# Kernel optimization log

Hardware: AMD Instinct MI355X
Metric: run time of the kernel (lower is better)

Reference implementation:

```python
import jax, jax.numpy as jnp
import numpy as np

N = 192            # image grid size (NxN)
N_SHOTS = 192
N_SAMPLES = 192
TWO_PI = 2.0 * np.pi
PIPE_ITERS = 3     # gpunufft default is ~10; 3 suffices for a CPU-runnable reference


def initialize_2D_radial(n_shots, n_samples):
    """Radial trajectory, k in [-0.5, 0.5), shape (n_shots*n_samples, 2)."""
    angles = np.pi * np.arange(n_shots) / n_shots
    radii = np.linspace(-0.5, 0.5, n_samples, endpoint=False)
    kx = radii[None, :] * np.cos(angles[:, None])
    ky = radii[None, :] * np.sin(angles[:, None])
    return np.stack([kx, ky], axis=-1).reshape(-1, 2).astype(np.float32)


def setup_inputs() -> dict:
    key = jax.random.key(0)
    x = jax.random.normal(key, (2, N, N), dtype=jnp.float32)  # real/imag image
    trajectory = jnp.asarray(initialize_2D_radial(N_SHOTS, N_SAMPLES))  # (M,2)
    return {"x": x, "trajectory": trajectory}


def _mats(traj):
    # Separable NDFT factors: exp(-2pi i k_x * px), exp(-2pi i k_y * py).
    # A: (M, N), B: (M, N); M*N complex64 ~= 57 MB each.
    p = jnp.arange(N, dtype=jnp.float32) - N / 2.0  # centered pixel coords
    A = jnp.exp(-1j * TWO_PI * traj[:, 0:1] * p[None, :])
    B = jnp.exp(-1j * TWO_PI * traj[:, 1:2] * p[None, :])
    return A.astype(jnp.complex64), B.astype(jnp.complex64)


def _op(img, A, B):
    # type-2 NUFFT (exact NDFT): image (N,N) -> kspace (M,)
    t = jnp.einsum('my,xy->mx', B, img)      # contract y first
    return jnp.einsum('mx,mx->m', A, t)


def _adj(d, A, B):
    # type-1 NUFFT adjoint: samples (M,) -> image (N,N)
    return jnp.einsum('mx,my->xy', jnp.conj(A) * d[:, None], jnp.conj(B))


def _pipe_density(A, B):
    # Pipe & Menon iterative density compensation: w <- w / |F F^H w|
    w = jnp.ones(A.shape[0], dtype=jnp.complex64)
    def body(i, w):
        q = _op(_adj(w, A, B), A, B)
        return w / jnp.maximum(jnp.abs(q), 1e-20)
    w = jax.lax.fori_loop(0, PIPE_ITERS, body, w)
    return jnp.abs(w)  # real positive weights


def reference(x, trajectory):
    img = (x[0] + 1j * x[1]).astype(jnp.complex64)  # (N,N) complex image
    A, B = _mats(trajectory)
    # density weights computed from detached trajectory (gpunufft init-time)
    traj_sg = jax.lax.stop_gradient(trajectory)
    Asg, Bsg = _mats(traj_sg)
    w = jax.lax.stop_gradient(_pipe_density(Asg, Bsg))
    kspace = _op(img, A, B)                       # forward NUFFT
    adjoint = _adj(w * kspace, A, B)              # density-compensated adjoint
    return jnp.stack([adjoint.real, adjoint.imag])  # (2,N,N) float32
```

## Files before the change

### kernel.cpp

```cpp
#include <hip/hip_runtime.h>
#include <math.h>


#define MTOT 36864
#define NPIX 192
#define SPLITS 128
#define MPS (MTOT / SPLITS)
#define ADJ_CHUNKS (MPS / 16)
#define PG 4

typedef __attribute__((ext_vector_type(8))) short s16x8;
typedef __attribute__((ext_vector_type(4))) float f32x4;
typedef __attribute__((ext_vector_type(4))) unsigned u32x4;

__device__ __forceinline__ f32x4 mfma_bf16(u32x4 a, u32x4 b, f32x4 c) {
    return __builtin_amdgcn_mfma_f32_16x16x32_bf16(
        __builtin_bit_cast(s16x8, a), __builtin_bit_cast(s16x8, b), c, 0, 0, 0);
}

__device__ __forceinline__ void g2l16(const void* g, void* l) {
    __builtin_amdgcn_global_load_lds(
        (const __attribute__((address_space(1))) void*)g,
        (__attribute__((address_space(3))) void*)l, 16, 0, 0);
}

__device__ __forceinline__ void split_pk(float a, float b, unsigned &hi, unsigned &lo) {
    const unsigned ua = __float_as_uint(a), ub = __float_as_uint(b);
    const unsigned ha = (ua + 0x8000u) & 0xffff0000u;
    const unsigned hb = (ub + 0x8000u) & 0xffff0000u;
    hi = (ha >> 16) | hb;
    const float la = a - __uint_as_float(ha);
    const float lb = b - __uint_as_float(hb);
    lo = ((__float_as_uint(la) + 0x8000u) >> 16) |
         ((__float_as_uint(lb) + 0x8000u) & 0xffff0000u);
}

__device__ __forceinline__ void ksplit(float k, float &kh, float &kl) {
    kh = __uint_as_float(__float_as_uint(k) & 0xfffff000u);
    kl = k - kh;
}
__device__ __forceinline__ float redphase(float kh, float kl, float p) {
    float r = kh * p;
    r -= rintf(r);
    r = fmaf(kl, p, r);
    return r;
}
__device__ __forceinline__ unsigned rot16(unsigned v) {
    return __builtin_amdgcn_alignbit(v, v, 16);
}
__device__ __forceinline__ int swz(int c) {
    return ((c ^ (c >> 2)) & 3) << 2;
}

__global__ void precompP_k(const float* __restrict__ traj, const int comp,
                           unsigned* __restrict__ PS) {
    const int m = blockIdx.x * 256 + threadIdx.x;
    const int c = blockIdx.y;
    float kh, kl; ksplit(traj[2 * m + comp], kh, kl);
    const float ph = redphase(kh, kl, (float)(c - 96));
    const float co = __builtin_amdgcn_cosf(ph);
    const float si = __builtin_amdgcn_sinf(ph);
    unsigned h, l; split_pk(co, -si, h, l);
    const int mc = m >> 4, mi = (m & 15) ^ swz(c);
    PS[(size_t)mc * 6144 + c * 16 + mi]        = h;
    PS[(size_t)mc * 6144 + 3072 + c * 16 + mi] = l;
}

__global__ void ebuild_k(const float* __restrict__ traj,
                         const float* __restrict__ dr, const float* __restrict__ di,
                         unsigned* __restrict__ ES) {
    const int m = blockIdx.x * 256 + threadIdx.x;
    const int c = blockIdx.y;
    float kh, kl; ksplit(traj[2 * m], kh, kl);
    const float ph = redphase(kh, kl, (float)(c - 96));
    const float co = __builtin_amdgcn_cosf(ph);
    const float si = __builtin_amdgcn_sinf(ph);
    const float dr_ = dr[m], di_ = di[m];
    const float Er = co * dr_ - si * di_;
    const float Ei = co * di_ + si * dr_;
    unsigned h, l; split_pk(Er, Ei, h, l);
    const int mc = m >> 4, mi = (m & 15) ^ swz(c);
    ES[(size_t)mc * 6144 + c * 16 + mi]        = h;
    ES[(size_t)mc * 6144 + 3072 + c * 16 + mi] = l;
}

__global__ void winit_k(float* __restrict__ wr, float* __restrict__ wi) {
    const int m = blockIdx.x * 256 + threadIdx.x;
    wr[m] = 1.f; wi[m] = 0.f;
}

__global__ __launch_bounds__(256) void adj_gemm_k(
    const unsigned* __restrict__ ES, const unsigned* __restrict__ BS,
    float* __restrict__ outP)
{
    __shared__ unsigned sAB[2][4096];
    const int tid = threadIdx.x;
    const int lane = tid & 63, wid = tid >> 6;
    const int l15 = lane & 15, qd = lane >> 4;
    const int L = blockIdx.x;
    const int xcd = L & 7, j = L >> 3;
    const int s = xcd * (SPLITS / 8) + j / 9;
    const int tile = j % 9;
    const int bx = tile % 3, by = tile / 3;
    const int wi = wid & 1, wj = wid >> 1;
    const int x0 = bx * 64 + wi * 32, y0 = by * 64 + wj * 32;
    float* outRe = outP + (size_t)(s & (PG - 1)) * (2 * MTOT);
    float* outIm = outRe + MTOT;

    f32x4 accRe[2][2], accIm[2][2];
    #pragma unroll
    for (int i = 0; i < 2; ++i)
        #pragma unroll
        for (int j2 = 0; j2 < 2; ++j2) {
            accRe[i][j2] = (f32x4){0.f, 0.f, 0.f, 0.f};
            accIm[i][j2] = (f32x4){0.f, 0.f, 0.f, 0.f};
        }

    const unsigned* gp[4];
    {
        const unsigned* E0 = ES + (size_t)(s * ADJ_CHUNKS) * 6144;
        const unsigned* B0 = BS + (size_t)(s * ADJ_CHUNKS) * 6144;
        gp[0] = E0 + bx * 1024 + tid * 4;
        gp[1] = E0 + 3072 + bx * 1024 + tid * 4;
        gp[2] = B0 + by * 1024 + tid * 4;
        gp[3] = B0 + 3072 + by * 1024 + tid * 4;
    }
    int eoff[2], boff[2];
    #pragma unroll
    for (int t = 0; t < 2; ++t) {
        const int cE = wi * 32 + t * 16 + l15;
        eoff[t] = cE * 16 + ((qd ^ ((cE ^ (cE >> 2)) & 3)) << 2);
        const int cB = wj * 32 + t * 16 + l15;
        boff[t] = 2048 + cB * 16 + ((qd ^ ((cB ^ (cB >> 2)) & 3)) << 2);
    }

    #pragma unroll
    for (int v = 0; v < 4; ++v)
        g2l16(gp[v], &sAB[0][v * 1024 + tid * 4]);
    __syncthreads();

    for (int ch = 0; ch < ADJ_CHUNKS; ++ch) {
        const int cur = ch & 1, nxt = cur ^ 1;
        if (ch + 1 < ADJ_CHUNKS) {
            #pragma unroll
            for (int v = 0; v < 4; ++v) {
                gp[v] += 6144;
                g2l16(gp[v], &sAB[nxt][v * 1024 + tid * 4]);
            }
        }

        u32x4 Eh[2], El[2];
        #pragma unroll
        for (int t = 0; t < 2; ++t) {
            Eh[t] = *(const u32x4*)(&sAB[cur][eoff[t]]);
            El[t] = *(const u32x4*)(&sAB[cur][1024 + eoff[t]]);
        }
        #pragma unroll
        for (int sj = 0; sj < 2; ++sj) {
            const u32x4 Ph = *(const u32x4*)(&sAB[cur][boff[sj]]);
            const u32x4 Pl = *(const u32x4*)(&sAB[cur][1024 + boff[sj]]);
            u32x4 Qh, Ql;
            #pragma unroll
            for (int r = 0; r < 4; ++r) {
                Qh[r] = rot16(Ph[r]) ^ 0x00008000u;
                Ql[r] = rot16(Pl[r]) ^ 0x00008000u;
            }
            #pragma unroll
            for (int si = 0; si < 2; ++si) {
                accRe[si][sj] = mfma_bf16(Eh[si], Ph, accRe[si][sj]);
                accRe[si][sj] = mfma_bf16(Eh[si], Pl, accRe[si][sj]);
                accRe[si][sj] = mfma_bf16(El[si], Ph, accRe[si][sj]);
                accIm[si][sj] = mfma_bf16(Eh[si], Qh, accIm[si][sj]);
                accIm[si][sj] = mfma_bf16(Eh[si], Ql, accIm[si][sj]);
                accIm[si][sj] = mfma_bf16(El[si], Qh, accIm[si][sj]);
            }
        }
        __syncthreads();
    }

    #pragma unroll
    for (int si = 0; si < 2; ++si)
        #pragma unroll
        for (int sj = 0; sj < 2; ++sj)
            #pragma unroll
            for (int rg = 0; rg < 4; ++rg) {
                const int x = x0 + si * 16 + qd * 4 + rg;
                const int y = y0 + sj * 16 + l15;
                atomicAdd(outRe + x * NPIX + y, accRe[si][sj][rg]);
                atomicAdd(outIm + x * NPIX + y, accIm[si][sj][rg]);
            }
}

__device__ __forceinline__ void fw_stage_load(const unsigned* __restrict__ Ghi,
                                              const unsigned* __restrict__ Glo,
                                              int tid, int koff, u32x4 st[3]) {
    #pragma unroll
    for (int j = 0; j < 3; ++j) {
        const int li = tid + j * 576;
        if (li < 1536) {
            const int row = li >> 3, pl = (li >> 2) & 1, qt = li & 3;
            const unsigned* src = pl ? Glo : Ghi;
            st[j] = *(const u32x4*)(src + row * 192 + koff + qt * 4);
        }
    }
}
__device__ __forceinline__ void fw_stage_write(unsigned* sb, int tid, const u32x4 st[3]) {
    #pragma unroll
    for (int j = 0; j < 3; ++j) {
        const int li = tid + j * 576;
        if (li < 1536) {
            const int row = li >> 3, pl = (li >> 2) & 1, qt = li & 3;
            *(u32x4*)(sb + pl * 3840 + row * 20 + qt * 4) = st[j];
        }
    }
}

__global__ __launch_bounds__(576) void fwdq_k(
    const float* __restrict__ traj,
    const unsigned* __restrict__ Ghi, const unsigned* __restrict__ Glo,
    float* __restrict__ wre, float* __restrict__ wim,
    const int mode,
    float* __restrict__ qre, float* __restrict__ qim)
{
    __shared__ unsigned sG[2][2 * 3840];
    const int tid = threadIdx.x;
    const int lane = tid & 63, wid = tid >> 6;
    const int l15 = lane & 15, q = lane >> 4;
    const int m = (blockIdx.x * 9 + wid) * 16 + l15;
    const float2 kk = *(const float2*)(traj + 2 * m);
    float kxh, kxl, kyh, kyl;
    ksplit(kk.x, kxh, kxl);
    ksplit(kk.y, kyh, kyl);

    f32x4 tre[12], tim[12];
    #pragma unroll
    for (int i = 0; i < 12; ++i) {
        tre[i] = (f32x4){0.f, 0.f, 0.f, 0.f};
        tim[i] = (f32x4){0.f, 0.f, 0.f, 0.f};
    }

    float bc, bs;
    { const float ph = redphase(kyh, kyl, (float)(q * 4 - 96)); 
      bc = __builtin_amdgcn_cosf(ph); bs = __builtin_amdgcn_sinf(ph); }
    const float r1c = __builtin_amdgcn_cosf(kk.y), r1s = __builtin_amdgcn_sinf(kk.y);
    float r16c, r16s;
    { float g = kk.y * 16.f; g -= rintf(g);
      r16c = __builtin_amdgcn_cosf(g); r16s = __builtin_amdgcn_sinf(g); }

    u32x4 st[3];
    fw_stage_load(Ghi, Glo, tid, 0, st);
    fw_stage_write(&sG[0][0], tid, st);
    __syncthreads();

    for (int ch = 0; ch < 12; ++ch) {
        if (ch < 11) fw_stage_load(Ghi, Glo, tid, (ch + 1) * 16, st);

        u32x4 Ph, Pl, Qh, Ql;
        {
            float c = bc, s = bs;
            #pragma unroll
            for (int r = 0; r < 4; ++r) {
                unsigned h, l; split_pk(c, s, h, l);
                Ph[r] = h; Pl[r] = l;
                Qh[r] = rot16(h) ^ 0x00008000u;
                Ql[r] = rot16(l) ^ 0x00008000u;
                const float nc = c * r1c - s * r1s, ns = s * r1c + c * r1s;
                c = nc; s = ns;
            }
            const float nbc = bc * r16c - bs * r16s, nbs = bs * r16c + bc * r16s;
            bc = nbc; bs = nbs;
        }

        const unsigned* sb = &sG[ch & 1][0];
        #pragma unroll
        for (int si = 0; si < 12; ++si) {
            const int base = (si * 16 + l15) * 20 + q * 4;
            const u32x4 gh = *(const u32x4*)(sb + base);
            const u32x4 gl = *(const u32x4*)(sb + 3840 + base);
            tre[si] = mfma_bf16(gh, Ph, tre[si]);
            tre[si] = mfma_bf16(gh, Pl, tre[si]);
            tre[si] = mfma_bf16(gl, Ph, tre[si]);
            tim[si] = mfma_bf16(gh, Qh, tim[si]);
            tim[si] = mfma_bf16(gh, Ql, tim[si]);
            tim[si] = mfma_bf16(gl, Qh, tim[si]);
        }

        if (ch < 11) {
            __syncthreads();
            fw_stage_write(&sG[(ch + 1) & 1][0], tid, st);
            __syncthreads();
        }
    }

    float qr = 0.f, qi = 0.f;
    {
        float g = kk.x * 16.f; g -= rintf(g);
        const float rc = __builtin_amdgcn_cosf(g), rs = __builtin_amdgcn_sinf(g);
        #pragma unroll
        for (int rg = 0; rg < 4; ++rg) {
            const float ph = redphase(kxh, kxl, (float)(q * 4 + rg - 96));
            float c = __builtin_amdgcn_cosf(ph), s = __builtin_amdgcn_sinf(ph);
            #pragma unroll
            for (int si = 0; si < 12; ++si) {
                const float tr = tre[si][rg], ti = tim[si][rg];
                qr += c * tr + s * ti;
                qi += c * ti - s * tr;
                const float nc = c * rc - s * rs, ns = s * rc + c * rs;
                c = nc; s = ns;
            }
        }
    }
    qr += __shfl_xor(qr, 16); qi += __shfl_xor(qi, 16);
    qr += __shfl_xor(qr, 32); qi += __shfl_xor(qi, 32);
    if (lane < 16) {
        if (mode == 0) {
            const float den = fmaxf(sqrtf(qr * qr + qi * qi), 1e-20f);
            wre[m] /= den; wim[m] /= den;
        } else {
            const float sc = sqrtf(wre[m] * wre[m] + wim[m] * wim[m]);
            qre[m] = qr * sc; qim[m] = qi * sc;
        }
    }
}

__global__ void presplit_k(const float* __restrict__ re, const float* __restrict__ im,
                           unsigned* __restrict__ Gh, unsigned* __restrict__ Gl) {
    const int e = blockIdx.x * 256 + threadIdx.x;
    unsigned h, l;
    split_pk(re[e], im[e], h, l);
    Gh[e] = h; Gl[e] = l;
}

__global__ void presplitP_k(const float* __restrict__ outP,
                            unsigned* __restrict__ Gh, unsigned* __restrict__ Gl) {
    const int e = blockIdx.x * 256 + threadIdx.x;
    float re = 0.f, im = 0.f;
    #pragma unroll
    for (int g = 0; g < PG; ++g) {
        re += outP[(size_t)g * (2 * MTOT) + e];
        im += outP[(size_t)g * (2 * MTOT) + MTOT + e];
    }
    unsigned h, l;
    split_pk(re, im, h, l);
    Gh[e] = h; Gl[e] = l;
}

__global__ void reduceOut_k(const float* __restrict__ outP, float* __restrict__ out) {
    const int e = blockIdx.x * 256 + threadIdx.x;
    float re = 0.f, im = 0.f;
    #pragma unroll
    for (int g = 0; g < PG; ++g) {
        re += outP[(size_t)g * (2 * MTOT) + e];
        im += outP[(size_t)g * (2 * MTOT) + MTOT + e];
    }
    out[e] = re; out[MTOT + e] = im;
}

extern "C" void kernel_launch(void* const* d_in, const int* in_sizes, int n_in,
                              void* d_out, int out_size, void* d_ws, size_t ws_size,
                              hipStream_t stream)
{
    const float* xin  = (const float*)d_in[0];
    const float* traj = (const float*)d_in[1];
    float* out = (float*)d_out;

    char* pb = (char*)d_ws;
    unsigned* BS = (unsigned*)pb; pb += (size_t)2304 * 6144 * 4;
    unsigned* ES = (unsigned*)pb; pb += (size_t)2304 * 6144 * 4;
    float* outP = (float*)pb; pb += (size_t)PG * 2 * MTOT * 4;
    float* wr   = (float*)pb; pb += MTOT * 4;
    float* wi   = (float*)pb; pb += MTOT * 4;
    float* dre  = (float*)pb; pb += MTOT * 4;
    float* dim_ = (float*)pb; pb += MTOT * 4;
    unsigned* Ghi = (unsigned*)pb; pb += MTOT * 4;
    unsigned* Glo = (unsigned*)pb; pb += MTOT * 4;

    precompP_k<<<dim3(MTOT / 256, NPIX), 256, 0, stream>>>(traj, 1, BS);
    winit_k<<<MTOT / 256, 256, 0, stream>>>(wr, wi);

    for (int it = 0; it < 3; ++it) {
        hipMemsetAsync(outP, 0, (size_t)PG * 2 * MTOT * 4, stream);
        ebuild_k<<<dim3(MTOT / 256, NPIX), 256, 0, stream>>>(traj, wr, wi, ES);
        adj_gemm_k<<<9 * SPLITS, 256, 0, stream>>>(ES, BS, outP);
        presplitP_k<<<MTOT / 256, 256, 0, stream>>>(outP, Ghi, Glo);
        fwdq_k<<<256, 576, 0, stream>>>(traj, Ghi, Glo, wr, wi, 0, dre, dim_);
    }

    presplit_k<<<MTOT / 256, 256, 0, stream>>>(xin, xin + MTOT, Ghi, Glo);
    fwdq_k<<<256, 576, 0, stream>>>(traj, Ghi, Glo, wr, wi, 1, dre, dim_);
    hipMemsetAsync(outP, 0, (size_t)PG * 2 * MTOT * 4, stream);
    ebuild_k<<<dim3(MTOT / 256, NPIX), 256, 0, stream>>>(traj, dre, dim_, ES);
    adj_gemm_k<<<9 * SPLITS, 256, 0, stream>>>(ES, BS, outP);
    reduceOut_k<<<MTOT / 256, 256, 0, stream>>>(outP, out);
}
```

Before: 491.2 us.

## Triple-buffer adjoint GEMM LDS tiles with explicit vmcnt waits

Moves the adjoint GEMM kernel from double-buffered to triple-buffered LDS staging, issuing global-to-LDS loads two chunks ahead. Each iteration waits only on the older loads through explicit vmcnt counts. All LDS fragments are read into registers before a second barrier, so the MFMA work runs after the buffer is released. The aim is to hide global load latency behind compute and remove the trailing full syncthreads. In exchange it uses more LDS per block, which may lower occupancy, and it relies on hand-written waitcnt values being correct.

```diff
diff --git a/kernel.cpp b/kernel.cpp
--- a/kernel.cpp
+++ b/kernel.cpp
@@ -93,7 +93,7 @@
     const unsigned* __restrict__ ES, const unsigned* __restrict__ BS,
     float* __restrict__ outP)
 {
-    __shared__ unsigned sAB[2][4096];
+    __shared__ unsigned sAB[3][4096];
     const int tid = threadIdx.x;
     const int lane = tid & 63, wid = tid >> 6;
     const int l15 = lane & 15, qd = lane >> 4;
@@ -137,28 +137,45 @@
     #pragma unroll
     for (int v = 0; v < 4; ++v)
         g2l16(gp[v], &sAB[0][v * 1024 + tid * 4]);
-    __syncthreads();
-
+    #pragma unroll
+    for (int v = 0; v < 4; ++v) {
+        gp[v] += 6144;
+        g2l16(gp[v], &sAB[1][v * 1024 + tid * 4]);
+    }
+
+    int rb = 0;
     for (int ch = 0; ch < ADJ_CHUNKS; ++ch) {
-        const int cur = ch & 1, nxt = cur ^ 1;
-        if (ch + 1 < ADJ_CHUNKS) {
+        if (ch + 2 < ADJ_CHUNKS) {
+            const int wb = (rb + 2 >= 3) ? rb - 1 : rb + 2;
             #pragma unroll
             for (int v = 0; v < 4; ++v) {
                 gp[v] += 6144;
-                g2l16(gp[v], &sAB[nxt][v * 1024 + tid * 4]);
-            }
-        }
-
-        u32x4 Eh[2], El[2];
+                g2l16(gp[v], &sAB[wb][v * 1024 + tid * 4]);
+            }
+            asm volatile("s_waitcnt vmcnt(8)" ::: "memory");
+        } else if (ch + 1 < ADJ_CHUNKS) {
+            asm volatile("s_waitcnt vmcnt(4)" ::: "memory");
+        } else {
+            asm volatile("s_waitcnt vmcnt(0)" ::: "memory");
+        }
+        __builtin_amdgcn_s_barrier();
+
+        const unsigned* sb = &sAB[rb][0];
+        u32x4 Eh[2], El[2], PhA[2], PlA[2];
         #pragma unroll
         for (int t = 0; t < 2; ++t) {
-            Eh[t] = *(const u32x4*)(&sAB[cur][eoff[t]]);
-            El[t] = *(const u32x4*)(&sAB[cur][1024 + eoff[t]]);
-        }
+            Eh[t]  = *(const u32x4*)(sb + eoff[t]);
+            El[t]  = *(const u32x4*)(sb + 1024 + eoff[t]);
+            PhA[t] = *(const u32x4*)(sb + boff[t]);
+            PlA[t] = *(const u32x4*)(sb + 1024 + boff[t]);
+        }
+        asm volatile("s_waitcnt lgkmcnt(0)" ::: "memory");
+        __builtin_amdgcn_sched_barrier(0);
+        __builtin_amdgcn_s_barrier();
+
         #pragma unroll
         for (int sj = 0; sj < 2; ++sj) {
-            const u32x4 Ph = *(const u32x4*)(&sAB[cur][boff[sj]]);
-            const u32x4 Pl = *(const u32x4*)(&sAB[cur][1024 + boff[sj]]);
+            const u32x4 Ph = PhA[sj], Pl = PlA[sj];
             u32x4 Qh, Ql;
             #pragma unroll
             for (int r = 0; r < 4; ++r) {
@@ -175,7 +192,7 @@
                 accIm[si][sj] = mfma_bf16(El[si], Qh, accIm[si][sj]);
             }
         }
-        __syncthreads();
+        rb = (rb + 1 == 3) ? 0 : rb + 1;
     }
 
     #pragma unroll
```

Measured after the change: 497.9 us. No clear change (+1.4%).

## Load adjoint GEMM operands directly from global into registers, dropping LDS staging

Applied to the files above, without the earlier changes.

The adjoint GEMM kernel stops staging E and P chunks through double-buffered LDS with global_load_lds and barriers. Each wave now loads its own MFMA fragments straight from global memory into registers, prefetching the next chunk into registers. The XOR swizzle in the precompute kernels is removed so the fragments sit contiguously, and launch bounds request 4 blocks per SM. This removes LDS traffic and per-chunk __syncthreads, but waves sharing a block tile now fetch overlapping data redundantly through cache, and register pressure rises.

```diff
diff --git a/kernel.cpp b/kernel.cpp
--- a/kernel.cpp
+++ b/kernel.cpp
@@ -16,12 +16,6 @@
 __device__ __forceinline__ f32x4 mfma_bf16(u32x4 a, u32x4 b, f32x4 c) {
     return __builtin_amdgcn_mfma_f32_16x16x32_bf16(
         __builtin_bit_cast(s16x8, a), __builtin_bit_cast(s16x8, b), c, 0, 0, 0);
-}
-
-__device__ __forceinline__ void g2l16(const void* g, void* l) {
-    __builtin_amdgcn_global_load_lds(
-        (const __attribute__((address_space(1))) void*)g,
-        (__attribute__((address_space(3))) void*)l, 16, 0, 0);
 }
 
 __device__ __forceinline__ void split_pk(float a, float b, unsigned &hi, unsigned &lo) {
@@ -48,9 +42,6 @@
 __device__ __forceinline__ unsigned rot16(unsigned v) {
     return __builtin_amdgcn_alignbit(v, v, 16);
 }
-__device__ __forceinline__ int swz(int c) {
-    return ((c ^ (c >> 2)) & 3) << 2;
-}
 
 __global__ void precompP_k(const float* __restrict__ traj, const int comp,
                            unsigned* __restrict__ PS) {
@@ -61,7 +52,7 @@
     const float co = __builtin_amdgcn_cosf(ph);
     const float si = __builtin_amdgcn_sinf(ph);
     unsigned h, l; split_pk(co, -si, h, l);
-    const int mc = m >> 4, mi = (m & 15) ^ swz(c);
+    const int mc = m >> 4, mi = m & 15;
     PS[(size_t)mc * 6144 + c * 16 + mi]        = h;
     PS[(size_t)mc * 6144 + 3072 + c * 16 + mi] = l;
 }
@@ -79,7 +70,7 @@
     const float Er = co * dr_ - si * di_;
     const float Ei = co * di_ + si * dr_;
     unsigned h, l; split_pk(Er, Ei, h, l);
-    const int mc = m >> 4, mi = (m & 15) ^ swz(c);
+    const int mc = m >> 4, mi = m & 15;
     ES[(size_t)mc * 6144 + c * 16 + mi]        = h;
     ES[(size_t)mc * 6144 + 3072 + c * 16 + mi] = l;
 }
@@ -89,11 +80,10 @@
     wr[m] = 1.f; wi[m] = 0.f;
 }
 
-__global__ __launch_bounds__(256) void adj_gemm_k(
+__global__ __launch_bounds__(256, 4) void adj_gemm_k(
     const unsigned* __restrict__ ES, const unsigned* __restrict__ BS,
     float* __restrict__ outP)
 {
-    __shared__ unsigned sAB[2][4096];
     const int tid = threadIdx.x;
     const int lane = tid & 63, wid = tid >> 6;
     const int l15 = lane & 15, qd = lane >> 4;
@@ -107,6 +97,15 @@
     float* outRe = outP + (size_t)(s & (PG - 1)) * (2 * MTOT);
     float* outIm = outRe + MTOT;
 
+    int eo0, eo1, bo0, bo1;
+    eo0 = (x0 + l15) * 16 + qd * 4;
+    eo1 = (x0 + 16 + l15) * 16 + qd * 4;
+    bo0 = (y0 + l15) * 16 + qd * 4;
+    bo1 = (y0 + 16 + l15) * 16 + qd * 4;
+
+    const unsigned* Ech = ES + (size_t)(s * ADJ_CHUNKS) * 6144;
+    const unsigned* Bch = BS + (size_t)(s * ADJ_CHUNKS) * 6144;
+
     f32x4 accRe[2][2], accIm[2][2];
     #pragma unroll
     for (int i = 0; i < 2; ++i)
@@ -116,49 +115,30 @@
             accIm[i][j2] = (f32x4){0.f, 0.f, 0.f, 0.f};
         }
 
-    const unsigned* gp[4];
-    {
-        const unsigned* E0 = ES + (size_t)(s * ADJ_CHUNKS) * 6144;
-        const unsigned* B0 = BS + (size_t)(s * ADJ_CHUNKS) * 6144;
-        gp[0] = E0 + bx * 1024 + tid * 4;
-        gp[1] = E0 + 3072 + bx * 1024 + tid * 4;
-        gp[2] = B0 + by * 1024 + tid * 4;
-        gp[3] = B0 + 3072 + by * 1024 + tid * 4;
-    }
-    int eoff[2], boff[2];
-    #pragma unroll
-    for (int t = 0; t < 2; ++t) {
-        const int cE = wi * 32 + t * 16 + l15;
-        eoff[t] = cE * 16 + ((qd ^ ((cE ^ (cE >> 2)) & 3)) << 2);
-        const int cB = wj * 32 + t * 16 + l15;
-        boff[t] = 2048 + cB * 16 + ((qd ^ ((cB ^ (cB >> 2)) & 3)) << 2);
-    }
-
-    #pragma unroll
-    for (int v = 0; v < 4; ++v)
-        g2l16(gp[v], &sAB[0][v * 1024 + tid * 4]);
-    __syncthreads();
-
-    for (int ch = 0; ch < ADJ_CHUNKS; ++ch) {
-        const int cur = ch & 1, nxt = cur ^ 1;
-        if (ch + 1 < ADJ_CHUNKS) {
-            #pragma unroll
-            for (int v = 0; v < 4; ++v) {
-                gp[v] += 6144;
-                g2l16(gp[v], &sAB[nxt][v * 1024 + tid * 4]);
-            }
-        }
-
-        u32x4 Eh[2], El[2];
-        #pragma unroll
-        for (int t = 0; t < 2; ++t) {
-            Eh[t] = *(const u32x4*)(&sAB[cur][eoff[t]]);
-            El[t] = *(const u32x4*)(&sAB[cur][1024 + eoff[t]]);
-        }
+    u32x4 cEh0 = *(const u32x4*)(Ech + eo0);
+    u32x4 cEh1 = *(const u32x4*)(Ech + eo1);
+    u32x4 cEl0 = *(const u32x4*)(Ech + 3072 + eo0);
+    u32x4 cEl1 = *(const u32x4*)(Ech + 3072 + eo1);
+    u32x4 cPh0 = *(const u32x4*)(Bch + bo0);
+    u32x4 cPh1 = *(const u32x4*)(Bch + bo1);
+    u32x4 cPl0 = *(const u32x4*)(Bch + 3072 + bo0);
+    u32x4 cPl1 = *(const u32x4*)(Bch + 3072 + bo1);
+
+    for (int ch = 0; ch < ADJ_CHUNKS - 1; ++ch) {
+        Ech += 6144; Bch += 6144;
+        u32x4 nEh0 = *(const u32x4*)(Ech + eo0);
+        u32x4 nEh1 = *(const u32x4*)(Ech + eo1);
+        u32x4 nEl0 = *(const u32x4*)(Ech + 3072 + eo0);
+        u32x4 nEl1 = *(const u32x4*)(Ech + 3072 + eo1);
+        u32x4 nPh0 = *(const u32x4*)(Bch + bo0);
+        u32x4 nPh1 = *(const u32x4*)(Bch + bo1);
+        u32x4 nPl0 = *(const u32x4*)(Bch + 3072 + bo0);
+        u32x4 nPl1 = *(const u32x4*)(Bch + 3072 + bo1);
+
         #pragma unroll
         for (int sj = 0; sj < 2; ++sj) {
-            const u32x4 Ph = *(const u32x4*)(&sAB[cur][boff[sj]]);
-            const u32x4 Pl = *(const u32x4*)(&sAB[cur][1024 + boff[sj]]);
+            const u32x4 Ph = sj ? cPh1 : cPh0;
+            const u32x4 Pl = sj ? cPl1 : cPl0;
             u32x4 Qh, Ql;
             #pragma unroll
             for (int r = 0; r < 4; ++r) {
@@ -167,15 +147,40 @@
             }
             #pragma unroll
             for (int si = 0; si < 2; ++si) {
-                accRe[si][sj] = mfma_bf16(Eh[si], Ph, accRe[si][sj]);
-                accRe[si][sj] = mfma_bf16(Eh[si], Pl, accRe[si][sj]);
-                accRe[si][sj] = mfma_bf16(El[si], Ph, accRe[si][sj]);
-                accIm[si][sj] = mfma_bf16(Eh[si], Qh, accIm[si][sj]);
-                accIm[si][sj] = mfma_bf16(Eh[si], Ql, accIm[si][sj]);
-                accIm[si][sj] = mfma_bf16(El[si], Qh, accIm[si][sj]);
+                const u32x4 Eh = si ? cEh1 : cEh0;
+                const u32x4 El = si ? cEl1 : cEl0;
+                accRe[si][sj] = mfma_bf16(Eh, Ph, accRe[si][sj]);
+                accRe[si][sj] = mfma_bf16(Eh, Pl, accRe[si][sj]);
+                accRe[si][sj] = mfma_bf16(El, Ph, accRe[si][sj]);
+                accIm[si][sj] = mfma_bf16(Eh, Qh, accIm[si][sj]);
+                accIm[si][sj] = mfma_bf16(Eh, Ql, accIm[si][sj]);
+                accIm[si][sj] = mfma_bf16(El, Qh, accIm[si][sj]);
             }
         }
-        __syncthreads();
+        cEh0 = nEh0; cEh1 = nEh1; cEl0 = nEl0; cEl1 = nEl1;
+        cPh0 = nPh0; cPh1 = nPh1; cPl0 = nPl0; cPl1 = nPl1;
+    }
+    #pragma unroll
+    for (int sj = 0; sj < 2; ++sj) {
+        const u32x4 Ph = sj ? cPh1 : cPh0;
+        const u32x4 Pl = sj ? cPl1 : cPl0;
+        u32x4 Qh, Ql;
+        #pragma unroll
+        for (int r = 0; r < 4; ++r) {
+            Qh[r] = rot16(Ph[r]) ^ 0x00008000u;
+            Ql[r] = rot16(Pl[r]) ^ 0x00008000u;
+        }
+        #pragma unroll
+        for (int si = 0; si < 2; ++si) {
+            const u32x4 Eh = si ? cEh1 : cEh0;
+            const u32x4 El = si ? cEl1 : cEl0;
+            accRe[si][sj] = mfma_bf16(Eh, Ph, accRe[si][sj]);
+            accRe[si][sj] = mfma_bf16(Eh, Pl, accRe[si][sj]);
+            accRe[si][sj] = mfma_bf16(El, Ph, accRe[si][sj]);
+            accIm[si][sj] = mfma_bf16(Eh, Qh, accIm[si][sj]);
+            accIm[si][sj] = mfma_bf16(Eh, Ql, accIm[si][sj]);
+            accIm[si][sj] = mfma_bf16(El, Qh, accIm[si][sj]);
+        }
     }
 
     #pragma unroll
```

Result: slower. 584.9 us (+19.1%).

## Replace LDS-staged adjoint GEMM with direct register-prefetched global loads per wave

Applied to the files above, without the earlier changes.

Each adjoint GEMM block becomes a single 64-thread wave that loads its E and B fragments straight from global memory into registers. A two-set register double buffer with sched_barrier separates prefetch from the MFMA work, replacing the LDS-staged global_load_lds pipeline and its per-chunk __syncthreads. The swizzle is removed from the producer kernels, since LDS bank conflicts no longer matter. Removing LDS traffic and barriers costs four times as many blocks, and each wave re-reads tiles that the old block shared through LDS, which raises L2 and global load traffic.

```diff
diff --git a/kernel.cpp b/kernel.cpp
--- a/kernel.cpp
+++ b/kernel.cpp
@@ -16,12 +16,6 @@
 __device__ __forceinline__ f32x4 mfma_bf16(u32x4 a, u32x4 b, f32x4 c) {
     return __builtin_amdgcn_mfma_f32_16x16x32_bf16(
         __builtin_bit_cast(s16x8, a), __builtin_bit_cast(s16x8, b), c, 0, 0, 0);
-}
-
-__device__ __forceinline__ void g2l16(const void* g, void* l) {
-    __builtin_amdgcn_global_load_lds(
-        (const __attribute__((address_space(1))) void*)g,
-        (__attribute__((address_space(3))) void*)l, 16, 0, 0);
 }
 
 __device__ __forceinline__ void split_pk(float a, float b, unsigned &hi, unsigned &lo) {
@@ -48,9 +42,6 @@
 __device__ __forceinline__ unsigned rot16(unsigned v) {
     return __builtin_amdgcn_alignbit(v, v, 16);
 }
-__device__ __forceinline__ int swz(int c) {
-    return ((c ^ (c >> 2)) & 3) << 2;
-}
 
 __global__ void precompP_k(const float* __restrict__ traj, const int comp,
                            unsigned* __restrict__ PS) {
@@ -61,7 +52,7 @@
     const float co = __builtin_amdgcn_cosf(ph);
     const float si = __builtin_amdgcn_sinf(ph);
     unsigned h, l; split_pk(co, -si, h, l);
-    const int mc = m >> 4, mi = (m & 15) ^ swz(c);
+    const int mc = m >> 4, mi = m & 15;
     PS[(size_t)mc * 6144 + c * 16 + mi]        = h;
     PS[(size_t)mc * 6144 + 3072 + c * 16 + mi] = l;
 }
@@ -79,7 +70,7 @@
     const float Er = co * dr_ - si * di_;
     const float Ei = co * di_ + si * dr_;
     unsigned h, l; split_pk(Er, Ei, h, l);
-    const int mc = m >> 4, mi = (m & 15) ^ swz(c);
+    const int mc = m >> 4, mi = m & 15;
     ES[(size_t)mc * 6144 + c * 16 + mi]        = h;
     ES[(size_t)mc * 6144 + 3072 + c * 16 + mi] = l;
 }
@@ -89,24 +80,31 @@
     wr[m] = 1.f; wi[m] = 0.f;
 }
 
-__global__ __launch_bounds__(256) void adj_gemm_k(
+__global__ __launch_bounds__(64, 4) void adj_gemm_k(
     const unsigned* __restrict__ ES, const unsigned* __restrict__ BS,
     float* __restrict__ outP)
 {
-    __shared__ unsigned sAB[2][4096];
-    const int tid = threadIdx.x;
-    const int lane = tid & 63, wid = tid >> 6;
+    const int lane = threadIdx.x & 63;
     const int l15 = lane & 15, qd = lane >> 4;
     const int L = blockIdx.x;
     const int xcd = L & 7, j = L >> 3;
-    const int s = xcd * (SPLITS / 8) + j / 9;
-    const int tile = j % 9;
+    const int s = xcd * (SPLITS / 8) + j / 36;
+    const int r = j % 36;
+    const int tile = r >> 2, wid = r & 3;
     const int bx = tile % 3, by = tile / 3;
     const int wi = wid & 1, wj = wid >> 1;
     const int x0 = bx * 64 + wi * 32, y0 = by * 64 + wj * 32;
     float* outRe = outP + (size_t)(s & (PG - 1)) * (2 * MTOT);
     float* outIm = outRe + MTOT;
 
+    const int eo0 = (x0 + l15) * 16 + qd * 4;
+    const int eo1 = (x0 + 16 + l15) * 16 + qd * 4;
+    const int bo0 = (y0 + l15) * 16 + qd * 4;
+    const int bo1 = (y0 + 16 + l15) * 16 + qd * 4;
+
+    const unsigned* Ep = ES + (size_t)(s * ADJ_CHUNKS) * 6144;
+    const unsigned* Bp = BS + (size_t)(s * ADJ_CHUNKS) * 6144;
+
     f32x4 accRe[2][2], accIm[2][2];
     #pragma unroll
     for (int i = 0; i < 2; ++i)
@@ -116,67 +114,65 @@
             accIm[i][j2] = (f32x4){0.f, 0.f, 0.f, 0.f};
         }
 
-    const unsigned* gp[4];
-    {
-        const unsigned* E0 = ES + (size_t)(s * ADJ_CHUNKS) * 6144;
-        const unsigned* B0 = BS + (size_t)(s * ADJ_CHUNKS) * 6144;
-        gp[0] = E0 + bx * 1024 + tid * 4;
-        gp[1] = E0 + 3072 + bx * 1024 + tid * 4;
-        gp[2] = B0 + by * 1024 + tid * 4;
-        gp[3] = B0 + 3072 + by * 1024 + tid * 4;
-    }
-    int eoff[2], boff[2];
-    #pragma unroll
-    for (int t = 0; t < 2; ++t) {
-        const int cE = wi * 32 + t * 16 + l15;
-        eoff[t] = cE * 16 + ((qd ^ ((cE ^ (cE >> 2)) & 3)) << 2);
-        const int cB = wj * 32 + t * 16 + l15;
-        boff[t] = 2048 + cB * 16 + ((qd ^ ((cB ^ (cB >> 2)) & 3)) << 2);
-    }
-
-    #pragma unroll
-    for (int v = 0; v < 4; ++v)
-        g2l16(gp[v], &sAB[0][v * 1024 + tid * 4]);
-    __syncthreads();
-
-    for (int ch = 0; ch < ADJ_CHUNKS; ++ch) {
-        const int cur = ch & 1, nxt = cur ^ 1;
-        if (ch + 1 < ADJ_CHUNKS) {
-            #pragma unroll
-            for (int v = 0; v < 4; ++v) {
-                gp[v] += 6144;
-                g2l16(gp[v], &sAB[nxt][v * 1024 + tid * 4]);
-            }
-        }
-
-        u32x4 Eh[2], El[2];
-        #pragma unroll
-        for (int t = 0; t < 2; ++t) {
-            Eh[t] = *(const u32x4*)(&sAB[cur][eoff[t]]);
-            El[t] = *(const u32x4*)(&sAB[cur][1024 + eoff[t]]);
-        }
-        #pragma unroll
-        for (int sj = 0; sj < 2; ++sj) {
-            const u32x4 Ph = *(const u32x4*)(&sAB[cur][boff[sj]]);
-            const u32x4 Pl = *(const u32x4*)(&sAB[cur][1024 + boff[sj]]);
-            u32x4 Qh, Ql;
-            #pragma unroll
-            for (int r = 0; r < 4; ++r) {
-                Qh[r] = rot16(Ph[r]) ^ 0x00008000u;
-                Ql[r] = rot16(Pl[r]) ^ 0x00008000u;
-            }
-            #pragma unroll
-            for (int si = 0; si < 2; ++si) {
-                accRe[si][sj] = mfma_bf16(Eh[si], Ph, accRe[si][sj]);
-                accRe[si][sj] = mfma_bf16(Eh[si], Pl, accRe[si][sj]);
-                accRe[si][sj] = mfma_bf16(El[si], Ph, accRe[si][sj]);
-                accIm[si][sj] = mfma_bf16(Eh[si], Qh, accIm[si][sj]);
-                accIm[si][sj] = mfma_bf16(Eh[si], Ql, accIm[si][sj]);
-                accIm[si][sj] = mfma_bf16(El[si], Qh, accIm[si][sj]);
-            }
-        }
-        __syncthreads();
-    }
+    u32x4 Ra[8], Rb[8];
+
+#define LOADSET(R)                                          \
+    R[0] = *(const u32x4*)(Ep + eo0);                       \
+    R[1] = *(const u32x4*)(Ep + eo1);                       \
+    R[2] = *(const u32x4*)(Ep + 3072 + eo0);                \
+    R[3] = *(const u32x4*)(Ep + 3072 + eo1);                \
+    R[4] = *(const u32x4*)(Bp + bo0);                       \
+    R[5] = *(const u32x4*)(Bp + bo1);                       \
+    R[6] = *(const u32x4*)(Bp + 3072 + bo0);                \
+    R[7] = *(const u32x4*)(Bp + 3072 + bo1);
+
+#define COMPUTE(R)                                                         \
+    {                                                                      \
+        _Pragma("unroll")                                                  \
+        for (int sj = 0; sj < 2; ++sj) {                                   \
+            const u32x4 Ph = R[4 + sj];                                    \
+            const u32x4 Pl = R[6 + sj];                                    \
+            u32x4 Qh, Ql;                                                  \
+            _Pragma("unroll")                                              \
+            for (int rr = 0; rr < 4; ++rr) {                               \
+                Qh[rr] = rot16(Ph[rr]) ^ 0x00008000u;                      \
+                Ql[rr] = rot16(Pl[rr]) ^ 0x00008000u;                      \
+            }                                                              \
+            _Pragma("unroll")                                              \
+            for (int si = 0; si < 2; ++si) {                               \
+                const u32x4 Eh = R[si];                                    \
+                const u32x4 El = R[2 + si];                                \
+                accRe[si][sj] = mfma_bf16(Eh, Ph, accRe[si][sj]);          \
+                accRe[si][sj] = mfma_bf16(Eh, Pl, accRe[si][sj]);          \
+                accRe[si][sj] = mfma_bf16(El, Ph, accRe[si][sj]);          \
+                accIm[si][sj] = mfma_bf16(Eh, Qh, accIm[si][sj]);          \
+                accIm[si][sj] = mfma_bf16(Eh, Ql, accIm[si][sj]);          \
+                accIm[si][sj] = mfma_bf16(El, Qh, accIm[si][sj]);          \
+            }                                                              \
+        }                                                                  \
+    }
+
+    LOADSET(Ra);
+    #pragma unroll 1
+    for (int it = 0; it < (ADJ_CHUNKS - 2) / 2; ++it) {
+        Ep += 6144; Bp += 6144;
+        LOADSET(Rb);
+        __builtin_amdgcn_sched_barrier(0);
+        COMPUTE(Ra);
+        Ep += 6144; Bp += 6144;
+        LOADSET(Ra);
+        __builtin_amdgcn_sched_barrier(0);
+        COMPUTE(Rb);
+    }
+    Ep += 6144; Bp += 6144;
+    LOADSET(Rb);
+    __builtin_amdgcn_sched_barrier(0);
+    COMPUTE(Ra);
+    __builtin_amdgcn_sched_barrier(0);
+    COMPUTE(Rb);
+
+#undef LOADSET
+#undef COMPUTE
 
     #pragma unroll
     for (int si = 0; si < 2; ++si)
@@ -381,7 +377,7 @@
     for (int it = 0; it < 3; ++it) {
         hipMemsetAsync(outP, 0, (size_t)PG * 2 * MTOT * 4, stream);
         ebuild_k<<<dim3(MTOT / 256, NPIX), 256, 0, stream>>>(traj, wr, wi, ES);
-        adj_gemm_k<<<9 * SPLITS, 256, 0, stream>>>(ES, BS, outP);
+        adj_gemm_k<<<36 * SPLITS, 64, 0, stream>>>(ES, BS, outP);
         presplitP_k<<<MTOT / 256, 256, 0, stream>>>(outP, Ghi, Glo);
         fwdq_k<<<256, 576, 0, stream>>>(traj, Ghi, Glo, wr, wi, 0, dre, dim_);
     }
@@ -390,6 +386,6 @@
     fwdq_k<<<256, 576, 0, stream>>>(traj, Ghi, Glo, wr, wi, 1, dre, dim_);
     hipMemsetAsync(outP, 0, (size_t)PG * 2 * MTOT * 4, stream);
     ebuild_k<<<dim3(MTOT / 256, NPIX), 256, 0, stream>>>(traj, dre, dim_, ES);
-    adj_gemm_k<<<9 * SPLITS, 256, 0, stream>>>(ES, BS, outP);
+    adj_gemm_k<<<36 * SPLITS, 64, 0, stream>>>(ES, BS, outP);
     reduceOut_k<<<MTOT / 256, 256, 0, stream>>>(outP, out);
 }
```

After: 528.3 us. +7.5%, slower.
